# Kernel tuning notes

Measured on AMD Instinct MI355X. Metric: run time of the kernel, lower is better.

## Reference

```python
import jax, jax.numpy as jnp
import numpy as np

B_, S_, F_, N_, H_ = 4, 8192, 512, 64, 2048  # batch, seq, features, state_dim, mlp hidden
EPS = 1e-5


def setup_inputs() -> dict:
    key = jax.random.key(0)
    ks = jax.random.split(key, 24)
    F, N, H = F_, N_, H_

    def nrm(k, shape, scale=1.0):
        return jax.random.normal(k, shape, dtype=jnp.float32) * scale

    inp = {}
    inp['x'] = nrm(ks[0], (B_, S_, F))
    inp['cond'] = nrm(ks[1], (B_, F))
    n = jnp.arange(N, dtype=jnp.float32)
    for i, p in enumerate(['fwd', 'bwd']):
        b = 2 + i * 6
        inp[p + '_logAre'] = jnp.log(n + 0.5)          # HiPPO-diag: A_real = -(n+0.5)
        inp[p + '_Aim'] = jnp.pi * n                    # HiPPO-diag: A_imag = pi*n
        inp[p + '_Bre'] = nrm(ks[b], (N, F), 1.0 / np.sqrt(N))
        inp[p + '_Bim'] = nrm(ks[b + 1], (N, F), 1.0 / np.sqrt(N))
        inp[p + '_Cre'] = nrm(ks[b + 2], (F, N), 1.0 / np.sqrt(F))
        inp[p + '_Cim'] = nrm(ks[b + 3], (F, N), 1.0 / np.sqrt(F))
        inp[p + '_D'] = nrm(ks[b + 4], (F,))
        inp[p + '_logdt'] = jax.random.uniform(ks[b + 5], (N,), minval=jnp.log(0.001), maxval=jnp.log(0.1))
    inp['proj_w'] = nrm(ks[14], (2 * F, F), 1.0 / np.sqrt(2 * F))
    inp['proj_b'] = jnp.zeros((F,), jnp.float32)
    # AdaLN modulation: Dense(6F) on silu(cond); zero-init in the model, small random here
    inp['ada_w'] = nrm(ks[15], (F, 6 * F), 0.02)
    inp['ada_b'] = jnp.zeros((6 * F,), jnp.float32)
    inp['mlp_w1'] = nrm(ks[16], (F, H), 1.0 / np.sqrt(F))
    inp['mlp_b1'] = jnp.zeros((H,), jnp.float32)
    inp['mlp_w2'] = nrm(ks[17], (H, F), 1.0 / np.sqrt(H))
    inp['mlp_b2'] = jnp.zeros((F,), jnp.float32)
    return inp


def _ln(x):
    mu = jnp.mean(x, axis=-1, keepdims=True)
    v = jnp.mean(jnp.square(x - mu), axis=-1, keepdims=True)
    return (x - mu) * jax.lax.rsqrt(v + EPS)


def _s5(u, logAre, Aim, Bre, Bim, Cre, Cim, D, logdt):
    dt = jnp.exp(logdt)
    A = -jnp.exp(logAre) + 1j * Aim                       # [N] complex diagonal
    A_bar = jnp.exp(A * dt)                               # ZOH discretization
    B_bar = (A_bar[:, None] - 1.0) / (A[:, None] + 1e-8) * (Bre + 1j * Bim)  # [N,F]
    u32 = u.astype(jnp.float32)
    Bu = jnp.einsum('bsf,nf->bsn', u32, B_bar)            # [B,S,N] complex
    Ab = jnp.broadcast_to(A_bar[None, None, :], Bu.shape)

    def op(e1, e2):
        a1, b1 = e1
        a2, b2 = e2
        return (a1 * a2, a2 * b1 + b2)

    _, xs = jax.lax.associative_scan(op, (Ab, Bu), axis=1)
    y = jnp.einsum('fn,bsn->bsf', Cre + 1j * Cim, xs).real + D * u32
    return y.astype(u.dtype)


def reference(x, cond, fwd_logAre, fwd_Aim, fwd_Bre, fwd_Bim, fwd_Cre, fwd_Cim, fwd_D, fwd_logdt,
              bwd_logAre, bwd_Aim, bwd_Bre, bwd_Bim, bwd_Cre, bwd_Cim, bwd_D, bwd_logdt,
              proj_w, proj_b, ada_w, ada_b, mlp_w1, mlp_b1, mlp_w2, mlp_b2):
    mods = jax.nn.silu(cond) @ ada_w + ada_b              # [B,6F]
    sh1, sc1, g1, sh2, sc2, g2 = [m[:, None, :] for m in jnp.split(mods, 6, axis=-1)]
    h = _ln(x) * (1.0 + sc1) + sh1
    y_fwd = _s5(h, fwd_logAre, fwd_Aim, fwd_Bre, fwd_Bim, fwd_Cre, fwd_Cim, fwd_D, fwd_logdt)
    y_bwd = jnp.flip(_s5(jnp.flip(h, axis=1), bwd_logAre, bwd_Aim, bwd_Bre, bwd_Bim, bwd_Cre, bwd_Cim, bwd_D, bwd_logdt), axis=1)
    y = jnp.concatenate([y_fwd, y_bwd], axis=-1) @ proj_w + proj_b
    x = x + g1 * y
    h2 = _ln(x) * (1.0 + sc2) + sh2
    x = x + g2 * (jax.nn.gelu(h2 @ mlp_w1 + mlp_b1) @ mlp_w2 + mlp_b2)
    return x
```

## Files before the change

kernel.cpp:

```cpp
#include <hip/hip_runtime.h>
#include <hip/hip_bf16.h>

typedef unsigned short u16;
typedef __attribute__((ext_vector_type(8))) short bf16x8;
typedef __attribute__((ext_vector_type(4))) float f32x4;

#define Bc 4
#define Sc 8192
#define Fc 512
#define Nc 64
#define Hc 2048
#define SIXF 3072

__device__ __forceinline__ u16 f2bf(float v) {
  __hip_bfloat16 h = __float2bfloat16(v);
  return *reinterpret_cast<u16*>(&h);
}
__device__ __forceinline__ float bf2f(u16 u) {
  return __uint_as_float(((unsigned)u) << 16);
}
__device__ __forceinline__ float ldf(const void* p, long i, int bf) {
  return bf ? bf2f(((const u16*)p)[i]) : ((const float*)p)[i];
}

__device__ __forceinline__ void ld16(const u16* g, u16* l) {
  __builtin_amdgcn_global_load_lds(
      (const __attribute__((address_space(1))) unsigned int*)g,
      (__attribute__((address_space(3))) unsigned int*)l,
      16, 0, 0);
}

__device__ __forceinline__ void xcd_swz(int& bx, int& by) {
  int gx = gridDim.x;
  int nwg = gx * gridDim.y;
  int lin = blockIdx.x + gx * blockIdx.y;
  if ((nwg & 7) == 0) {
    int q = nwg >> 3;
    lin = (lin & 7) * q + (lin >> 3);
  }
  bx = lin % gx;
  by = lin / gx;
}

__global__ void k_detect(const u16* __restrict__ x, int* __restrict__ flag) {
  if (threadIdx.x == 0) {
    int cnt = 0;
    for (int i = 0; i < 256; ++i) {
      int e = (x[i] >> 7) & 0xFF;
      cnt += (e >= 130);
    }
    *flag = (cnt >= 16) ? 0 : 1;
  }
}

__global__ void k_convert(const void* __restrict__ src, float* __restrict__ dst,
                          int n, const int* __restrict__ flag) {
  int bf = *flag;
  int i = blockIdx.x * blockDim.x + threadIdx.x;
  int stride = gridDim.x * blockDim.x;
  for (int j = i; j < n; j += stride) dst[j] = ldf(src, j, bf);
}

__global__ __launch_bounds__(256) void k_mods_init(const void* __restrict__ ada_b,
                                                   const int* __restrict__ flag,
                                                   float* __restrict__ mods) {
  int bf = *flag;
  int col = blockIdx.x * 256 + threadIdx.x;
  float v = ldf(ada_b, col, bf);
  for (int b = 0; b < Bc; ++b) mods[b * SIXF + col] = v;
}

__global__ __launch_bounds__(256) void k_mods2(const void* __restrict__ cond,
                                               const void* __restrict__ ada_w,
                                               const int* __restrict__ flag,
                                               float* __restrict__ mods) {
  int bf = *flag;
  int b = blockIdx.y;
  int f0 = blockIdx.z * 128;
  int col = blockIdx.x * 256 + threadIdx.x;
  __shared__ float sc[128];
  for (int i = threadIdx.x; i < 128; i += 256) {
    float c = ldf(cond, b * Fc + f0 + i, bf);
    sc[i] = c / (1.f + expf(-c));
  }
  __syncthreads();
  float acc = 0.f;
  for (int f = 0; f < 128; ++f) acc = fmaf(sc[f], ldf(ada_w, (long)(f0 + f) * SIXF + col, bf), acc);
  atomicAdd(&mods[b * SIXF + col], acc);
}

__global__ void k_prep(const void* lAf, const void* Aif, const void* Brf, const void* Bif, const void* ldtf,
                       const void* lAb, const void* Aib, const void* Brb, const void* Bib, const void* ldtb,
                       const int* __restrict__ flag,
                       u16* __restrict__ Wbup, float* __restrict__ Abar) {
  int bf = *flag;
  int dir = blockIdx.x;
  int f0 = blockIdx.y * 64;
  int n = threadIdx.x;
  const void* lA = dir ? lAb : lAf;
  const void* Ai = dir ? Aib : Aif;
  const void* Br = dir ? Brb : Brf;
  const void* Bi = dir ? Bib : Bif;
  const void* ld = dir ? ldtb : ldtf;
  float dt  = expf(ldf(ld, n, bf));
  float Are = -expf(ldf(lA, n, bf));
  float Aim = ldf(Ai, n, bf);
  float er  = expf(Are * dt);
  float abr = er * cosf(Aim * dt);
  float abi = er * sinf(Aim * dt);
  if (blockIdx.y == 0) {
    Abar[(dir * Nc + n) * 2 + 0] = abr;
    Abar[(dir * Nc + n) * 2 + 1] = abi;
  }
  float dr = Are + 1e-8f, di = Aim;
  float den = dr * dr + di * di;
  float nr = abr - 1.f, ni = abi;
  float cr = (nr * dr + ni * di) / den;
  float ci = (ni * dr - nr * di) / den;
  int col_re = dir * 128 + n, col_im = dir * 128 + 64 + n;
  for (int f = f0; f < f0 + 64; ++f) {
    float br = ldf(Br, n * Fc + f, bf), bi = ldf(Bi, n * Fc + f, bf);
    Wbup[(((f >> 3) * 256) + col_re) * 8 + (f & 7)] = f2bf(cr * br - ci * bi);
    Wbup[(((f >> 3) * 256) + col_im) * 8 + (f & 7)] = f2bf(cr * bi + ci * br);
  }
}

__global__ __launch_bounds__(256) void k_P2p(const void* Df, const void* Db, const void* pw,
                                             const int* __restrict__ flag, u16* __restrict__ Wyp) {
  int bf = *flag;
  int idx = blockIdx.x * 256 + threadIdx.x;
  int f1 = idx >> 9, fo = idx & 511;
  float v = ldf(Df, f1, bf) * ldf(pw, (long)f1 * Fc + fo, bf) +
            ldf(Db, f1, bf) * ldf(pw, (long)(Fc + f1) * Fc + fo, bf);
  Wyp[((((f1 >> 3) + 64) * Fc) + fo) * 8 + (f1 & 7)] = f2bf(v);
}

__global__ __launch_bounds__(256) void k_Cpm(const void* Cref, const void* Cimf,
                                             const void* Creb, const void* Cimb,
                                             const int* __restrict__ flag, u16* __restrict__ Cpm) {
  int bf = *flag;
  int k = blockIdx.x;
  int dir = k >> 7, c = (k >> 6) & 1, n = k & 63;
  const void* C = dir ? (c ? Cimb : Creb) : (c ? Cimf : Cref);
  float sgn = c ? -1.f : 1.f;
  for (int f = threadIdx.x; f < Fc; f += 256)
    Cpm[k * Fc + f] = f2bf(sgn * ldf(C, (long)f * Nc + n, bf));
}

__global__ __launch_bounds__(256) void k_Wpack(const void* __restrict__ src, const int* __restrict__ flag,
                                               int log2N, u16* __restrict__ dst) {
  int bf = *flag;
  long i = (long)blockIdx.x * 256 + threadIdx.x;
  int Nn = 1 << log2N;
  long k8 = i >> log2N;
  int n = (int)(i & (Nn - 1));
  u16 tmp[8];
#pragma unroll
  for (int j = 0; j < 8; ++j)
    tmp[j] = f2bf(ldf(src, ((k8 << 3) + j) * (long)Nn + n, bf));
  *(ushort4*)(dst + i * 8)     = *(ushort4*)tmp;
  *(ushort4*)(dst + i * 8 + 4) = *(ushort4*)(tmp + 4);
}

__global__ __launch_bounds__(256) void k_ln(const void* __restrict__ src, int srcmode,
                                            long src_tok_base, int b0,
                                            const int* __restrict__ flag,
                                            const float* __restrict__ mods,
                                            int sh_base, int sc_base,
                                            u16* __restrict__ dst, int ldd, int dcol) {
  int bf = srcmode ? 1 : *flag;
  long lt = blockIdx.x;
  int b = b0 + (int)(lt >> 13);
  int t = threadIdx.x;
  long si = (src_tok_base + lt) * Fc;
  float x0 = ldf(src, si + t, bf);
  float x1 = ldf(src, si + t + 256, bf);
  float s = x0 + x1, qq = x0 * x0 + x1 * x1;
  for (int o = 32; o; o >>= 1) { s += __shfl_down(s, o); qq += __shfl_down(qq, o); }
  __shared__ float ss[4], sq[4];
  int w = t >> 6;
  if ((t & 63) == 0) { ss[w] = s; sq[w] = qq; }
  __syncthreads();
  float S = ss[0] + ss[1] + ss[2] + ss[3];
  float Q = sq[0] + sq[1] + sq[2] + sq[3];
  float mu = S * (1.f / Fc);
  float var = Q * (1.f / Fc) - mu * mu;
  float rs = rsqrtf(var + 1e-5f);
  const float* mb = mods + b * SIXF;
  float h0 = (x0 - mu) * rs * (1.f + mb[sc_base + t]) + mb[sh_base + t];
  float h1 = (x1 - mu) * rs * (1.f + mb[sc_base + t + 256]) + mb[sh_base + t + 256];
  dst[lt * (long)ldd + dcol + t] = f2bf(h0);
  dst[lt * (long)ldd + dcol + t + 256] = f2bf(h1);
}

struct SmemA { u16 As[2][128 * 64]; u16 Ws[2][64 * 128]; };

__device__ __forceinline__ void mfma_gemm128(SmemA& sm, const u16* __restrict__ A, long row0,
                                             int lda, int K,
                                             const u16* __restrict__ Wp, int N, int col0,
                                             f32x4 (&acc)[4][4]) {
  const int tid = threadIdx.x;
  const int l = tid & 63, q = l >> 4, li = l & 15;
  const int w = tid >> 6;
  const int wm = (w >> 1) << 6, wn = (w & 1) << 6;
  const int m0 = tid >> 3;
  const int kc0 = (tid & 7) ^ (m0 & 7);
  const long aoff0 = (row0 + m0) * (long)lda + (kc0 << 3);
  const long woff0 = (long)(tid >> 7) * ((long)N << 3) + ((long)(col0 + (tid & 127)) << 3);
  const int lb = w << 9;
  const int T = K >> 6;
  int cur = 0;
  auto stage = [&](int buf, int k0) {
#pragma unroll
    for (int it = 0; it < 4; ++it)
      ld16(A + aoff0 + (long)it * ((long)lda << 5) + k0, sm.As[buf] + (it << 11) + lb);
#pragma unroll
    for (int it = 0; it < 4; ++it)
      ld16(Wp + woff0 + (long)k0 * N + (long)it * ((long)N << 4), sm.Ws[buf] + (it << 11) + lb);
  };
  stage(0, 0);
  for (int t = 0; t < T; ++t) {
    if (t + 1 < T) {
      stage(cur ^ 1, (t + 1) << 6);
      asm volatile("s_waitcnt vmcnt(8)" ::: "memory");
    } else {
      asm volatile("s_waitcnt vmcnt(0)" ::: "memory");
    }
    __builtin_amdgcn_s_barrier();
    __builtin_amdgcn_sched_barrier(0);
    const u16* As = sm.As[cur];
    const u16* Ws = sm.Ws[cur];
#pragma unroll
    for (int ks = 0; ks < 2; ++ks) {
      bf16x8 af[4], bw[4];
#pragma unroll
      for (int mt = 0; mt < 4; ++mt) {
        int mrow = wm + (mt << 4) + li;
        af[mt] = *(const bf16x8*)(As + (((mrow << 3) + (((ks << 2) + q) ^ (mrow & 7))) << 3));
      }
#pragma unroll
      for (int nt = 0; nt < 4; ++nt) {
        int n = wn + (nt << 4) + li;
        bw[nt] = *(const bf16x8*)(Ws + (((((ks << 2) + q) << 7) | n) << 3));
      }
#pragma unroll
      for (int mt = 0; mt < 4; ++mt)
#pragma unroll
        for (int nt = 0; nt < 4; ++nt)
          acc[mt][nt] = __builtin_amdgcn_mfma_f32_16x16x32_bf16(af[mt], bw[nt], acc[mt][nt], 0, 0, 0);
    }
    __builtin_amdgcn_s_barrier();
    __builtin_amdgcn_sched_barrier(0);
    cur ^= 1;
  }
}

struct SmemC { u16 As[4][256 * 32]; u16 Ws[4][32 * 256]; };

__device__ __forceinline__ void mfma_gemm256(SmemC& sm, const u16* __restrict__ A, long row0,
                                             int lda, int K,
                                             const u16* __restrict__ Wp, int N, int col0,
                                             f32x4 (&acc)[8][4]) {
  const int tid = threadIdx.x;
  const int l = tid & 63, q = l >> 4, li = l & 15;
  const int w = tid >> 6;
  const int wm = (w >> 2) << 7, wn = (w & 3) << 6;
  const int m0 = tid >> 2;
  const int kc0 = (tid & 3) ^ ((tid >> 3) & 3);
  const long aoff0 = (row0 + m0) * (long)lda + (kc0 << 3);
  const long woff0 = (long)(tid >> 8) * ((long)N << 3) + ((long)(col0 + (tid & 255)) << 3);
  const int T = K >> 5;
  auto stage = [&](int buf, int t) {
    const int k0 = t << 5;
#pragma unroll
    for (int it = 0; it < 2; ++it)
      ld16(A + aoff0 + (long)(it << 7) * lda + k0, sm.As[buf] + (((it << 9) + tid) << 3));
#pragma unroll
    for (int it = 0; it < 2; ++it)
      ld16(Wp + woff0 + (((long)((k0 >> 3) + (it << 1)) * N) << 3),
           sm.Ws[buf] + (((it << 9) + tid) << 3));
  };
  stage(0, 0); stage(1, 1); stage(2, 2);
  for (int t = 0; t < T; ++t) {
    if (t + 3 < T) stage((t + 3) & 3, t + 3);
    int rem = T - 1 - t;
    if (rem >= 3)      asm volatile("s_waitcnt vmcnt(12)" ::: "memory");
    else if (rem == 2) asm volatile("s_waitcnt vmcnt(8)" ::: "memory");
    else if (rem == 1) asm volatile("s_waitcnt vmcnt(4)" ::: "memory");
    else               asm volatile("s_waitcnt vmcnt(0)" ::: "memory");
    __builtin_amdgcn_s_barrier();
    __builtin_amdgcn_sched_barrier(0);
    const u16* As = sm.As[t & 3];
    const u16* Ws = sm.Ws[t & 3];
    __builtin_amdgcn_s_setprio(1);
    bf16x8 bw[4];
#pragma unroll
    for (int nt = 0; nt < 4; ++nt) {
      int n = wn + (nt << 4) + li;
      bw[nt] = *(const bf16x8*)(Ws + (((q << 8) | n) << 3));
    }
#pragma unroll
    for (int mt = 0; mt < 8; ++mt) {
      int mrow = wm + (mt << 4) + li;
      bf16x8 af = *(const bf16x8*)(As + (((mrow << 2) + (q ^ ((mrow >> 1) & 3))) << 3));
#pragma unroll
      for (int nt = 0; nt < 4; ++nt)
        acc[mt][nt] = __builtin_amdgcn_mfma_f32_16x16x32_bf16(af, bw[nt], acc[mt][nt], 0, 0, 0);
    }
    __builtin_amdgcn_s_setprio(0);
    __builtin_amdgcn_s_barrier();
    __builtin_amdgcn_sched_barrier(0);
  }
}

__global__ __launch_bounds__(256) void k_Gp2(const u16* __restrict__ Cpm, const u16* __restrict__ pwp,
                                             u16* __restrict__ Wyp) {
  __shared__ SmemA sm;
  f32x4 acc[4][4] = {};
  int bx, by; xcd_swz(bx, by);
  long row0 = (long)by * 128;
  int col0 = bx << 7;
  int dir = (int)(row0 >> 7);
  mfma_gemm128(sm, Cpm, row0, Fc, Fc, pwp + (size_t)dir * 262144, Fc, col0, acc);
  const int l = threadIdx.x & 63, q = l >> 4, li = l & 15;
  const int w = threadIdx.x >> 6;
  const int wm = (w >> 1) << 6, wn = (w & 1) << 6;
#pragma unroll
  for (int mt = 0; mt < 4; ++mt)
#pragma unroll
    for (int nt = 0; nt < 4; ++nt)
#pragma unroll
      for (int r = 0; r < 4; ++r) {
        int k = (int)row0 + wm + (mt << 4) + (q << 2) + r;
        int col = col0 + wn + (nt << 4) + li;
        u16 v = f2bf(acc[mt][nt][r]);
        size_t i0 = (((size_t)(k >> 3)) * Fc + col) * 8 + (k & 7);
        Wyp[i0] = v;
        Wyp[i0 + (size_t)32 * Fc * 8] = v;
      }
}

__global__ __launch_bounds__(256) void k_gemm_bu(const u16* __restrict__ hp,
                                                 const u16* __restrict__ Wbup,
                                                 int nb, float* __restrict__ Bu) {
  __shared__ SmemA sm;
  f32x4 acc[4][4] = {};
  int bx, by; xcd_swz(bx, by);
  long row0 = (long)by * 128;
  int col0 = bx << 7;
  mfma_gemm128(sm, hp, row0, 1024, Fc, Wbup, 256, col0, acc);
  const int l = threadIdx.x & 63, q = l >> 4, li = l & 15;
  const int w = threadIdx.x >> 6;
  const int wm = (w >> 1) << 6, wn = (w & 1) << 6;
#pragma unroll
  for (int mt = 0; mt < 4; ++mt) {
#pragma unroll
    for (int nt = 0; nt < 4; ++nt) {
      int col = col0 + wn + (nt << 4) + li;
      int dir = col >> 7, cc = (col >> 6) & 1, n = col & 63;
#pragma unroll
      for (int r = 0; r < 4; ++r) {
        long lt = row0 + wm + (mt << 4) + (q << 2) + r;
        int lb = (int)(lt >> 13), s = (int)(lt & 8191);
        int spos = dir ? (Sc - 1 - s) : s;
        Bu[((((long)dir * nb + lb) * Nc + n) * Sc + spos) * 2 + cc] = acc[mt][nt][r];
      }
    }
  }
}

__global__ __launch_bounds__(256) void k_scan(float* __restrict__ Bu, const float* __restrict__ Abar,
                                              int nb) {
  int blk = blockIdx.x;
  int per_dir = nb * 64;
  int dir = blk / per_dir;
  int rem = blk - dir * per_dir;
  int lb = rem >> 6, n = rem & 63;
  float ar = Abar[(dir * Nc + n) * 2 + 0];
  float ai = Abar[(dir * Nc + n) * 2 + 1];
  float* base = Bu + (((long)dir * nb + lb) * Nc + n) * Sc * 2;
  int t = threadIdx.x;
  float4 loc[16];
  float lr = 0.f, li = 0.f;
  const float4* bp = (const float4*)base + t * 16;
#pragma unroll
  for (int j = 0; j < 16; ++j) {
    float4 v = bp[j];
    loc[j] = v;
    float nr = fmaf(ar, lr, fmaf(-ai, li, v.x));
    float ni = fmaf(ar, li, fmaf(ai, lr, v.y));
    lr = fmaf(ar, nr, fmaf(-ai, ni, v.z));
    li = fmaf(ar, ni, fmaf(ai, nr, v.w));
  }
  __shared__ float sr[256], si[256];
  float pr = ar, pi = ai;
  for (int k = 0; k < 5; ++k) { float t2 = pr * pr - pi * pi; pi = 2.f * pr * pi; pr = t2; }
  float vr = lr, vi = li;
  for (int step = 1; step < 256; step <<= 1) {
    sr[t] = vr; si[t] = vi;
    __syncthreads();
    if (t >= step) {
      float orr = sr[t - step], oii = si[t - step];
      vr = vr + pr * orr - pi * oii;
      vi = vi + pr * oii + pi * orr;
    }
    __syncthreads();
    float t2 = pr * pr - pi * pi; pi = 2.f * pr * pi; pr = t2;
  }
  sr[t] = vr; si[t] = vi;
  __syncthreads();
  float xr = (t == 0) ? 0.f : sr[t - 1];
  float xi = (t == 0) ? 0.f : si[t - 1];
  float4* op = (float4*)base + t * 16;
#pragma unroll
  for (int j = 0; j < 16; ++j) {
    float4 v = loc[j];
    float nr = fmaf(ar, xr, fmaf(-ai, xi, v.x));
    float ni = fmaf(ar, xi, fmaf(ai, xr, v.y));
    xr = fmaf(ar, nr, fmaf(-ai, ni, v.z));
    xi = fmaf(ar, ni, fmaf(ai, nr, v.w));
    float4 o; o.x = nr; o.y = ni; o.z = xr; o.w = xi;
    op[j] = o;
  }
}

__global__ __launch_bounds__(256) void k_xs_t(const float* __restrict__ xs, int nb,
                                              u16* __restrict__ hxl) {
  __shared__ float tile[32 * 257];
  long t0 = (long)blockIdx.x * 32;
  int lb = (int)(t0 >> 13);
  int s0 = (int)(t0 & 8191);
  int tid = threadIdx.x;
  int ls = tid & 31;
  int half = (tid >> 5) & 1;
  int wv = tid >> 6;
#pragma unroll 4
  for (int cg = 0; cg < 32; ++cg) {
    int col = cg * 8 + wv * 2 + half;
    int dir = col >> 7, cc = (col >> 6) & 1, n = col & 63;
    int spos = dir ? (Sc - 1 - (s0 + ls)) : (s0 + ls);
    float v = xs[((((long)dir * nb + lb) * Nc + n) * Sc + spos) * 2 + cc];
    tile[ls * 257 + col] = v;
  }
  __syncthreads();
  for (int j = 0; j < 32; ++j) {
    float v = tile[j * 257 + tid];
    u16 hi = f2bf(v);
    long lt = t0 + j;
    hxl[lt * 1024 + tid] = hi;
    hxl[lt * 1024 + 256 + tid] = f2bf(v - bf2f(hi));
  }
}

__global__ __launch_bounds__(512, 2) void k_gemm_y(const u16* __restrict__ hxl,
                                                   const u16* __restrict__ Wyp,
                                                   const void* __restrict__ xraw, long tok_base, int b0,
                                                   const int* __restrict__ flag,
                                                   const float* __restrict__ mods,
                                                   const float* __restrict__ pb,
                                                   u16* __restrict__ out1) {
  __shared__ SmemC sm;
  f32x4 acc[8][4] = {};
  int bx, by; xcd_swz(bx, by);
  long row0 = (long)by << 8;
  int col0 = bx << 8;
  mfma_gemm256(sm, hxl, row0, 1024, 1024, Wyp, Fc, col0, acc);
  int bf = *flag;
  const int l = threadIdx.x & 63, q = l >> 4, li = l & 15;
  const int w = threadIdx.x >> 6;
  const int wm = (w >> 2) << 7, wn = (w & 3) << 6;
#pragma unroll
  for (int mt = 0; mt < 8; ++mt) {
#pragma unroll
    for (int r = 0; r < 4; ++r) {
      long lt = row0 + wm + (mt << 4) + (q << 2) + r;
      int b = b0 + (int)(lt >> 13);
      const float* mb = mods + b * SIXF + 2 * Fc;
#pragma unroll
      for (int nt = 0; nt < 4; ++nt) {
        int col = col0 + wn + (nt << 4) + li;
        float xv = ldf(xraw, (tok_base + lt) * Fc + col, bf);
        out1[lt * Fc + col] = f2bf(xv + mb[col] * (acc[mt][nt][r] + pb[col]));
      }
    }
  }
}

__device__ __forceinline__ float gelu_t(float u) {
  float z = 0.7978845608028654f * fmaf(0.044715f * u * u, u, u);
  float e = __builtin_amdgcn_exp2f(z * -2.8853900817779268f);
  return u * __builtin_amdgcn_rcpf(1.f + e);
}

__global__ __launch_bounds__(512, 2) void k_mlp1(const u16* __restrict__ h2, const u16* __restrict__ W1p,
                                                 const float* __restrict__ b1, long crow0,
                                                 u16* __restrict__ tbuf) {
  __shared__ SmemC sm;
  f32x4 acc[8][4] = {};
  int bx, by; xcd_swz(bx, by);
  long row0 = crow0 + ((long)by << 8);
  int col0 = bx << 8;
  mfma_gemm256(sm, h2, row0, Fc, Fc, W1p, Hc, col0, acc);
  const int l = threadIdx.x & 63, q = l >> 4, li = l & 15;
  const int w = threadIdx.x >> 6;
  const int wm = (w >> 2) << 7, wn = (w & 3) << 6;
#pragma unroll
  for (int mt = 0; mt < 8; ++mt) {
#pragma unroll
    for (int r = 0; r < 4; ++r) {
      long lr2 = row0 - crow0 + wm + (mt << 4) + (q << 2) + r;
#pragma unroll
      for (int nt = 0; nt < 4; ++nt) {
        int col = col0 + wn + (nt << 4) + li;
        tbuf[lr2 * Hc + col] = f2bf(gelu_t(acc[mt][nt][r] + b1[col]));
      }
    }
  }
}

__global__ __launch_bounds__(256) void k_mlp2(const u16* __restrict__ tbuf, const u16* __restrict__ W2p,
                                              const float* __restrict__ b2, const u16* __restrict__ out1,
                                              const float* __restrict__ mods, long crow0,
                                              long tok_base, int b0,
                                              const int* __restrict__ flag, void* __restrict__ dout) {
  __shared__ SmemA sm;
  f32x4 acc[4][4] = {};
  int bx, by; xcd_swz(bx, by);
  long lrow0 = (long)by * 128;
  int col0 = bx << 7;
  mfma_gemm128(sm, tbuf, lrow0, Hc, Hc, W2p, Fc, col0, acc);
  int bf = *flag;
  const int l = threadIdx.x & 63, q = l >> 4, li = l & 15;
  const int w = threadIdx.x >> 6;
  const int wm = (w >> 1) << 6, wn = (w & 1) << 6;
#pragma unroll
  for (int mt = 0; mt < 4; ++mt) {
#pragma unroll
    for (int r = 0; r < 4; ++r) {
      long lt = crow0 + lrow0 + wm + (mt << 4) + (q << 2) + r;
      int b = b0 + (int)(lt >> 13);
      const float* mb = mods + b * SIXF + 5 * Fc;
#pragma unroll
      for (int nt = 0; nt < 4; ++nt) {
        int col = col0 + wn + (nt << 4) + li;
        float v = bf2f(out1[lt * Fc + col]) + mb[col] * (acc[mt][nt][r] + b2[col]);
        long oi = (tok_base + lt) * Fc + col;
        if (bf) ((u16*)dout)[oi] = f2bf(v);
        else    ((float*)dout)[oi] = v;
      }
    }
  }
}

extern "C" void kernel_launch(void* const* d_in, const int* in_sizes, int n_in,
                              void* d_out, int out_size, void* d_ws, size_t ws_size,
                              hipStream_t stream) {
  char* ws = (char*)d_ws;
  size_t off = 0;
  auto alloc = [&](size_t bytes) -> char* {
    char* p = ws + off;
    off += (bytes + 255) & ~(size_t)255;
    return p;
  };
  int*   flag = (int*)  alloc(4);
  float* mods = (float*)alloc((size_t)Bc * SIXF * 4);
  float* Abar = (float*)alloc(2 * Nc * 2 * 4);
  float* pbf  = (float*)alloc(Fc * 4);
  float* b1f  = (float*)alloc(Hc * 4);
  float* b2f  = (float*)alloc(Fc * 4);
  u16* Wbup = (u16*)alloc((size_t)Fc * 256 * 2);
  u16* Wyp  = (u16*)alloc((size_t)128 * Fc * 8 * 2);
  u16* W1p  = (u16*)alloc((size_t)Fc * Hc * 2);
  u16* W2p  = (u16*)alloc((size_t)Hc * Fc * 2);
  u16* pwp  = (u16*)alloc((size_t)1024 * Fc * 2);
  u16* Cpm  = (u16*)alloc((size_t)256 * Fc * 2);
  size_t off_static = off;

  const size_t U = (size_t)Sc * Fc * 2;
  int nb = 4;
  while (nb > 1 && off_static + (size_t)nb * 4 * U + 4096 > ws_size) nb >>= 1;

  u16*   hxl  = (u16*)  alloc((size_t)nb * U * 2);
  float* Bu   = (float*)alloc((size_t)nb * U);
  u16*   out1 = (u16*)  alloc((size_t)nb * U);
  u16* tch = hxl;
  u16* h2  = (u16*)Bu;

  k_detect<<<1, 64, 0, stream>>>((const u16*)d_in[0], flag);
  k_convert<<<2, 256, 0, stream>>>(d_in[19], pbf, Fc, flag);
  k_convert<<<8, 256, 0, stream>>>(d_in[23], b1f, Hc, flag);
  k_convert<<<2, 256, 0, stream>>>(d_in[25], b2f, Fc, flag);
  k_mods_init<<<12, 256, 0, stream>>>(d_in[21], flag, mods);
  k_mods2<<<dim3(12, Bc, 4), 256, 0, stream>>>(d_in[1], d_in[20], flag, mods);
  k_prep<<<dim3(2, 8), 64, 0, stream>>>(d_in[2], d_in[3], d_in[4], d_in[5], d_in[9],
                                        d_in[10], d_in[11], d_in[12], d_in[13], d_in[17],
                                        flag, Wbup, Abar);
  k_P2p<<<(Fc * Fc) / 256, 256, 0, stream>>>(d_in[8], d_in[16], d_in[18], flag, Wyp);
  k_Wpack<<<256, 256, 0, stream>>>(d_in[18], flag, 9, pwp);
  k_Cpm<<<256, 256, 0, stream>>>(d_in[6], d_in[7], d_in[14], d_in[15], flag, Cpm);
  k_Gp2<<<dim3(4, 2), 256, 0, stream>>>(Cpm, pwp, Wyp);
  k_Wpack<<<512, 256, 0, stream>>>(d_in[22], flag, 11, W1p);
  k_Wpack<<<512, 256, 0, stream>>>(d_in[24], flag, 9, W2p);

  for (int b0 = 0; b0 < Bc; b0 += nb) {
    long tok_base = (long)b0 * Sc;
    long rows = (long)nb * Sc;
    k_ln<<<rows, 256, 0, stream>>>(d_in[0], 0, tok_base, b0, flag, mods, 0, Fc, hxl, 1024, 512);
    k_gemm_bu<<<dim3(2, rows / 128), 256, 0, stream>>>(hxl + 512, Wbup, nb, Bu);
    k_scan<<<2 * nb * 64, 256, 0, stream>>>(Bu, Abar, nb);
    k_xs_t<<<rows / 32, 256, 0, stream>>>(Bu, nb, hxl);
    k_gemm_y<<<dim3(2, rows / 256), 512, 0, stream>>>(hxl, Wyp, d_in[0], tok_base, b0,
                                                      flag, mods, pbf, out1);
    k_ln<<<rows, 256, 0, stream>>>(out1, 1, 0, b0, flag, mods, 3 * Fc, 4 * Fc, h2, 512, 0);
    long RC = rows / 2;
    for (int ch = 0; ch < 2; ++ch) {
      long crow0 = ch * RC;
      k_mlp1<<<dim3(8, RC / 256), 512, 0, stream>>>(h2, W1p, b1f, crow0, tch);
      k_mlp2<<<dim3(4, RC / 128), 256, 0, stream>>>(tch, W2p, b2f, out1, mods, crow0,
                                                    tok_base, b0, flag, d_out);
    }
  }
  (void)n_in; (void)out_size; (void)in_sizes;
}
```

Before: 621.6 us.

## Restructure GEMM pipelines to one barrier per K-step and add BK=64 MLP1 path

Each GEMM main loop now waits for its loads, issues a single barrier, and only then starts the next prefetch, dropping the trailing barrier per iteration. In the 128 GEMM the prefetch is no longer overlapped with the wait because it waits on vmcnt(0). A new 256x256 GEMM with BK=64 and double buffering (128 KB of shared memory) is added for the MLP1 kernel, replacing the 4-stage BK=32 pipeline there. The larger LDS footprint may keep two blocks per CU from fitting, and the shallower prefetch can expose memory latency.

After: 628.4 us. Within noise of the previous version (+1.1%).

```diff
diff --git a/kernel.cpp b/kernel.cpp
--- a/kernel.cpp
+++ b/kernel.cpp
@@ -193,6 +193,7 @@
   dst[lt * (long)ldd + dcol + t + 256] = f2bf(h1);
 }
 
+
 struct SmemA { u16 As[2][128 * 64]; u16 Ws[2][64 * 128]; };
 
 __device__ __forceinline__ void mfma_gemm128(SmemA& sm, const u16* __restrict__ A, long row0,
@@ -220,14 +221,10 @@
   };
   stage(0, 0);
   for (int t = 0; t < T; ++t) {
-    if (t + 1 < T) {
-      stage(cur ^ 1, (t + 1) << 6);
-      asm volatile("s_waitcnt vmcnt(8)" ::: "memory");
-    } else {
-      asm volatile("s_waitcnt vmcnt(0)" ::: "memory");
-    }
+    asm volatile("s_waitcnt vmcnt(0)" ::: "memory");
     __builtin_amdgcn_s_barrier();
     __builtin_amdgcn_sched_barrier(0);
+    if (t + 1 < T) stage(cur ^ 1, (t + 1) << 6);
     const u16* As = sm.As[cur];
     const u16* Ws = sm.Ws[cur];
 #pragma unroll
@@ -249,18 +246,72 @@
         for (int nt = 0; nt < 4; ++nt)
           acc[mt][nt] = __builtin_amdgcn_mfma_f32_16x16x32_bf16(af[mt], bw[nt], acc[mt][nt], 0, 0, 0);
     }
+    cur ^= 1;
+  }
+}
+
+struct SmemB { u16 As[2][256 * 64]; u16 Ws[2][64 * 256]; };
+
+__device__ __forceinline__ void mfma_gemm256b(SmemB& sm, const u16* __restrict__ A, long row0,
+                                              int lda, int K,
+                                              const u16* __restrict__ Wp, int N, int col0,
+                                              f32x4 (&acc)[8][4]) {
+  const int tid = threadIdx.x;
+  const int l = tid & 63, q = l >> 4, li = l & 15;
+  const int w = tid >> 6;
+  const int wm = (w >> 2) << 7, wn = (w & 3) << 6;
+  const int m0 = tid >> 3;
+  const int kc0 = (tid & 7) ^ (m0 & 7);
+  const long aoff0 = (row0 + m0) * (long)lda + (kc0 << 3);
+  const long woff0 = (long)(tid >> 8) * ((long)N << 3) + ((long)(col0 + (tid & 255)) << 3);
+  const int lb = w << 9;
+  const int T = K >> 6;
+  int cur = 0;
+  auto stage = [&](int buf, int k0) {
+#pragma unroll
+    for (int it = 0; it < 4; ++it)
+      ld16(A + aoff0 + (long)it * ((long)lda << 6) + k0, sm.As[buf] + (it << 12) + lb);
+#pragma unroll
+    for (int it = 0; it < 4; ++it)
+      ld16(Wp + woff0 + (long)k0 * N + (long)it * ((long)N << 4), sm.Ws[buf] + (it << 12) + lb);
+  };
+  stage(0, 0);
+  for (int t = 0; t < T; ++t) {
+    asm volatile("s_waitcnt vmcnt(0)" ::: "memory");
     __builtin_amdgcn_s_barrier();
     __builtin_amdgcn_sched_barrier(0);
+    if (t + 1 < T) stage(cur ^ 1, (t + 1) << 6);
+    const u16* As = sm.As[cur];
+    const u16* Ws = sm.Ws[cur];
+    __builtin_amdgcn_s_setprio(1);
+#pragma unroll
+    for (int ks = 0; ks < 2; ++ks) {
+      bf16x8 bw[4];
+#pragma unroll
+      for (int nt = 0; nt < 4; ++nt) {
+        int n = wn + (nt << 4) + li;
+        bw[nt] = *(const bf16x8*)(Ws + (((((ks << 2) + q) << 8) | n) << 3));
+      }
+#pragma unroll
+      for (int mt = 0; mt < 8; ++mt) {
+        int mrow = wm + (mt << 4) + li;
+        bf16x8 af = *(const bf16x8*)(As + (((mrow << 3) + (((ks << 2) + q) ^ (mrow & 7))) << 3));
+#pragma unroll
+        for (int nt = 0; nt < 4; ++nt)
+          acc[mt][nt] = __builtin_amdgcn_mfma_f32_16x16x32_bf16(af, bw[nt], acc[mt][nt], 0, 0, 0);
+      }
+    }
+    __builtin_amdgcn_s_setprio(0);
     cur ^= 1;
   }
 }
 
 struct SmemC { u16 As[4][256 * 32]; u16 Ws[4][32 * 256]; };
 
-__device__ __forceinline__ void mfma_gemm256(SmemC& sm, const u16* __restrict__ A, long row0,
-                                             int lda, int K,
-                                             const u16* __restrict__ Wp, int N, int col0,
-                                             f32x4 (&acc)[8][4]) {
+__device__ __forceinline__ void mfma_gemm256c(SmemC& sm, const u16* __restrict__ A, long row0,
+                                              int lda, int K,
+                                              const u16* __restrict__ Wp, int N, int col0,
+                                              f32x4 (&acc)[8][4]) {
   const int tid = threadIdx.x;
   const int l = tid & 63, q = l >> 4, li = l & 15;
   const int w = tid >> 6;
@@ -282,14 +333,13 @@
   };
   stage(0, 0); stage(1, 1); stage(2, 2);
   for (int t = 0; t < T; ++t) {
-    if (t + 3 < T) stage((t + 3) & 3, t + 3);
     int rem = T - 1 - t;
-    if (rem >= 3)      asm volatile("s_waitcnt vmcnt(12)" ::: "memory");
-    else if (rem == 2) asm volatile("s_waitcnt vmcnt(8)" ::: "memory");
+    if (rem >= 2)      asm volatile("s_waitcnt vmcnt(8)" ::: "memory");
     else if (rem == 1) asm volatile("s_waitcnt vmcnt(4)" ::: "memory");
     else               asm volatile("s_waitcnt vmcnt(0)" ::: "memory");
     __builtin_amdgcn_s_barrier();
     __builtin_amdgcn_sched_barrier(0);
+    if (t + 3 < T) stage((t + 3) & 3, t + 3);
     const u16* As = sm.As[t & 3];
     const u16* Ws = sm.Ws[t & 3];
     __builtin_amdgcn_s_setprio(1);
@@ -308,8 +358,6 @@
         acc[mt][nt] = __builtin_amdgcn_mfma_f32_16x16x32_bf16(af, bw[nt], acc[mt][nt], 0, 0, 0);
     }
     __builtin_amdgcn_s_setprio(0);
-    __builtin_amdgcn_s_barrier();
-    __builtin_amdgcn_sched_barrier(0);
   }
 }
 
@@ -464,7 +512,7 @@
   int bx, by; xcd_swz(bx, by);
   long row0 = (long)by << 8;
   int col0 = bx << 8;
-  mfma_gemm256(sm, hxl, row0, 1024, 1024, Wyp, Fc, col0, acc);
+  mfma_gemm256c(sm, hxl, row0, 1024, 1024, Wyp, Fc, col0, acc);
   int bf = *flag;
   const int l = threadIdx.x & 63, q = l >> 4, li = l & 15;
   const int w = threadIdx.x >> 6;
@@ -495,12 +543,12 @@
 __global__ __launch_bounds__(512, 2) void k_mlp1(const u16* __restrict__ h2, const u16* __restrict__ W1p,
                                                  const float* __restrict__ b1, long crow0,
                                                  u16* __restrict__ tbuf) {
-  __shared__ SmemC sm;
+  __shared__ SmemB sm;
   f32x4 acc[8][4] = {};
   int bx, by; xcd_swz(bx, by);
   long row0 = crow0 + ((long)by << 8);
   int col0 = bx << 8;
-  mfma_gemm256(sm, h2, row0, Fc, Fc, W1p, Hc, col0, acc);
+  mfma_gemm256b(sm, h2, row0, Fc, Fc, W1p, Hc, col0, acc);
   const int l = threadIdx.x & 63, q = l >> 4, li = l & 15;
   const int w = threadIdx.x >> 6;
   const int wm = (w >> 2) << 7, wn = (w & 3) << 6;
```

## Shrink big GEMM tiles to 128x256 with triple buffering and single barrier

Applied to the files above, without the earlier changes.

Replaces the 256x256 tile, 512-thread GEMM used by the y-projection and first MLP layer with a 128x256 tile on 256 threads, where each wave owns a 64-column strip across all 128 rows. It uses a 3-deep LDS ring with the next stage issued after the barrier, and drops the trailing barrier per K step. The 128x128 GEMM loop is also reordered: it waits for all loads, barriers, then prefetches the next buffer, so one barrier per iteration is removed. The aim is less barrier overhead and smaller LDS per block for better occupancy. The cost is less reuse per tile and, in the 128 GEMM, a full vmcnt(0) wait that serialises load and compute more.

New measurement: 624.5 us. No clear change (+0.5%).

```diff
diff --git a/kernel.cpp b/kernel.cpp
--- a/kernel.cpp
+++ b/kernel.cpp
@@ -193,6 +193,7 @@
   dst[lt * (long)ldd + dcol + t + 256] = f2bf(h1);
 }
 
+
 struct SmemA { u16 As[2][128 * 64]; u16 Ws[2][64 * 128]; };
 
 __device__ __forceinline__ void mfma_gemm128(SmemA& sm, const u16* __restrict__ A, long row0,
@@ -220,14 +221,10 @@
   };
   stage(0, 0);
   for (int t = 0; t < T; ++t) {
-    if (t + 1 < T) {
-      stage(cur ^ 1, (t + 1) << 6);
-      asm volatile("s_waitcnt vmcnt(8)" ::: "memory");
-    } else {
-      asm volatile("s_waitcnt vmcnt(0)" ::: "memory");
-    }
+    asm volatile("s_waitcnt vmcnt(0)" ::: "memory");
     __builtin_amdgcn_s_barrier();
     __builtin_amdgcn_sched_barrier(0);
+    if (t + 1 < T) stage(cur ^ 1, (t + 1) << 6);
     const u16* As = sm.As[cur];
     const u16* Ws = sm.Ws[cur];
 #pragma unroll
@@ -249,49 +246,44 @@
         for (int nt = 0; nt < 4; ++nt)
           acc[mt][nt] = __builtin_amdgcn_mfma_f32_16x16x32_bf16(af[mt], bw[nt], acc[mt][nt], 0, 0, 0);
     }
-    __builtin_amdgcn_s_barrier();
-    __builtin_amdgcn_sched_barrier(0);
     cur ^= 1;
   }
 }
 
-struct SmemC { u16 As[4][256 * 32]; u16 Ws[4][32 * 256]; };
-
-__device__ __forceinline__ void mfma_gemm256(SmemC& sm, const u16* __restrict__ A, long row0,
-                                             int lda, int K,
-                                             const u16* __restrict__ Wp, int N, int col0,
-                                             f32x4 (&acc)[8][4]) {
+struct SmemD { u16 As[3][128 * 32]; u16 Ws[3][32 * 256]; };
+
+__device__ __forceinline__ void mfma_gemmD(SmemD& sm, const u16* __restrict__ A, long row0,
+                                           int lda, int K,
+                                           const u16* __restrict__ Wp, int N, int col0,
+                                           f32x4 (&acc)[8][4]) {
   const int tid = threadIdx.x;
   const int l = tid & 63, q = l >> 4, li = l & 15;
   const int w = tid >> 6;
-  const int wm = (w >> 2) << 7, wn = (w & 3) << 6;
+  const int wn = w << 6;
   const int m0 = tid >> 2;
   const int kc0 = (tid & 3) ^ ((tid >> 3) & 3);
   const long aoff0 = (row0 + m0) * (long)lda + (kc0 << 3);
-  const long woff0 = (long)(tid >> 8) * ((long)N << 3) + ((long)(col0 + (tid & 255)) << 3);
+  const long woff0 = ((long)(col0 + tid)) << 3;
   const int T = K >> 5;
   auto stage = [&](int buf, int t) {
     const int k0 = t << 5;
-#pragma unroll
-    for (int it = 0; it < 2; ++it)
-      ld16(A + aoff0 + (long)(it << 7) * lda + k0, sm.As[buf] + (((it << 9) + tid) << 3));
-#pragma unroll
-    for (int it = 0; it < 2; ++it)
-      ld16(Wp + woff0 + (((long)((k0 >> 3) + (it << 1)) * N) << 3),
-           sm.Ws[buf] + (((it << 9) + tid) << 3));
+    ld16(A + aoff0 + k0, sm.As[buf] + (tid << 3));
+    ld16(A + aoff0 + ((long)lda << 6) + k0, sm.As[buf] + ((tid + 256) << 3));
+#pragma unroll
+    for (int j = 0; j < 4; ++j)
+      ld16(Wp + woff0 + (((long)((k0 >> 3) + j) * N) << 3),
+           sm.Ws[buf] + (((j << 8) + tid) << 3));
   };
-  stage(0, 0); stage(1, 1); stage(2, 2);
+  stage(0, 0);
+  if (T > 1) stage(1, 1);
   for (int t = 0; t < T; ++t) {
-    if (t + 3 < T) stage((t + 3) & 3, t + 3);
-    int rem = T - 1 - t;
-    if (rem >= 3)      asm volatile("s_waitcnt vmcnt(12)" ::: "memory");
-    else if (rem == 2) asm volatile("s_waitcnt vmcnt(8)" ::: "memory");
-    else if (rem == 1) asm volatile("s_waitcnt vmcnt(4)" ::: "memory");
-    else               asm volatile("s_waitcnt vmcnt(0)" ::: "memory");
+    if (t + 1 < T) asm volatile("s_waitcnt vmcnt(6)" ::: "memory");
+    else           asm volatile("s_waitcnt vmcnt(0)" ::: "memory");
     __builtin_amdgcn_s_barrier();
     __builtin_amdgcn_sched_barrier(0);
-    const u16* As = sm.As[t & 3];
-    const u16* Ws = sm.Ws[t & 3];
+    if (t + 2 < T) stage((t + 2) % 3, t + 2);
+    const u16* As = sm.As[t % 3];
+    const u16* Ws = sm.Ws[t % 3];
     __builtin_amdgcn_s_setprio(1);
     bf16x8 bw[4];
 #pragma unroll
@@ -301,15 +293,13 @@
     }
 #pragma unroll
     for (int mt = 0; mt < 8; ++mt) {
-      int mrow = wm + (mt << 4) + li;
+      int mrow = (mt << 4) + li;
       bf16x8 af = *(const bf16x8*)(As + (((mrow << 2) + (q ^ ((mrow >> 1) & 3))) << 3));
 #pragma unroll
       for (int nt = 0; nt < 4; ++nt)
         acc[mt][nt] = __builtin_amdgcn_mfma_f32_16x16x32_bf16(af, bw[nt], acc[mt][nt], 0, 0, 0);
     }
     __builtin_amdgcn_s_setprio(0);
-    __builtin_amdgcn_s_barrier();
-    __builtin_amdgcn_sched_barrier(0);
   }
 }
 
@@ -452,28 +442,27 @@
   }
 }
 
-__global__ __launch_bounds__(512, 2) void k_gemm_y(const u16* __restrict__ hxl,
+__global__ __launch_bounds__(256, 2) void k_gemm_y(const u16* __restrict__ hxl,
                                                    const u16* __restrict__ Wyp,
                                                    const void* __restrict__ xraw, long tok_base, int b0,
                                                    const int* __restrict__ flag,
                                                    const float* __restrict__ mods,
                                                    const float* __restrict__ pb,
                                                    u16* __restrict__ out1) {
-  __shared__ SmemC sm;
+  __shared__ SmemD sm;
   f32x4 acc[8][4] = {};
   int bx, by; xcd_swz(bx, by);
-  long row0 = (long)by << 8;
+  long row0 = (long)by << 7;
   int col0 = bx << 8;
-  mfma_gemm256(sm, hxl, row0, 1024, 1024, Wyp, Fc, col0, acc);
+  mfma_gemmD(sm, hxl, row0, 1024, 1024, Wyp, Fc, col0, acc);
   int bf = *flag;
   const int l = threadIdx.x & 63, q = l >> 4, li = l & 15;
-  const int w = threadIdx.x >> 6;
-  const int wm = (w >> 2) << 7, wn = (w & 3) << 6;
+  const int wn = (threadIdx.x >> 6) << 6;
 #pragma unroll
   for (int mt = 0; mt < 8; ++mt) {
 #pragma unroll
     for (int r = 0; r < 4; ++r) {
-      long lt = row0 + wm + (mt << 4) + (q << 2) + r;
+      long lt = row0 + (mt << 4) + (q << 2) + r;
       int b = b0 + (int)(lt >> 13);
       const float* mb = mods + b * SIXF + 2 * Fc;
 #pragma unroll
@@ -492,23 +481,22 @@
   return u * __builtin_amdgcn_rcpf(1.f + e);
 }
 
-__global__ __launch_bounds__(512, 2) void k_mlp1(const u16* __restrict__ h2, const u16* __restrict__ W1p,
+__global__ __launch_bounds__(256, 2) void k_mlp1(const u16* __restrict__ h2, const u16* __restrict__ W1p,
                                                  const float* __restrict__ b1, long crow0,
                                                  u16* __restrict__ tbuf) {
-  __shared__ SmemC sm;
+  __shared__ SmemD sm;
   f32x4 acc[8][4] = {};
   int bx, by; xcd_swz(bx, by);
-  long row0 = crow0 + ((long)by << 8);
+  long row0 = crow0 + ((long)by << 7);
   int col0 = bx << 8;
-  mfma_gemm256(sm, h2, row0, Fc, Fc, W1p, Hc, col0, acc);
+  mfma_gemmD(sm, h2, row0, Fc, Fc, W1p, Hc, col0, acc);
   const int l = threadIdx.x & 63, q = l >> 4, li = l & 15;
-  const int w = threadIdx.x >> 6;
-  const int wm = (w >> 2) << 7, wn = (w & 3) << 6;
+  const int wn = (threadIdx.x >> 6) << 6;
 #pragma unroll
   for (int mt = 0; mt < 8; ++mt) {
 #pragma unroll
     for (int r = 0; r < 4; ++r) {
-      long lr2 = row0 - crow0 + wm + (mt << 4) + (q << 2) + r;
+      long lr2 = row0 - crow0 + (mt << 4) + (q << 2) + r;
 #pragma unroll
       for (int nt = 0; nt < 4; ++nt) {
         int col = col0 + wn + (nt << 4) + li;
@@ -609,13 +597,13 @@
     k_gemm_bu<<<dim3(2, rows / 128), 256, 0, stream>>>(hxl + 512, Wbup, nb, Bu);
     k_scan<<<2 * nb * 64, 256, 0, stream>>>(Bu, Abar, nb);
     k_xs_t<<<rows / 32, 256, 0, stream>>>(Bu, nb, hxl);
-    k_gemm_y<<<dim3(2, rows / 256), 512, 0, stream>>>(hxl, Wyp, d_in[0], tok_base, b0,
+    k_gemm_y<<<dim3(2, rows / 128), 256, 0, stream>>>(hxl, Wyp, d_in[0], tok_base, b0,
                                                       flag, mods, pbf, out1);
     k_ln<<<rows, 256, 0, stream>>>(out1, 1, 0, b0, flag, mods, 3 * Fc, 4 * Fc, h2, 512, 0);
     long RC = rows / 2;
     for (int ch = 0; ch < 2; ++ch) {
       long crow0 = ch * RC;
-      k_mlp1<<<dim3(8, RC / 256), 512, 0, stream>>>(h2, W1p, b1f, crow0, tch);
+      k_mlp1<<<dim3(8, RC / 128), 256, 0, stream>>>(h2, W1p, b1f, crow0, tch);
       k_mlp2<<<dim3(4, RC / 128), 256, 0, stream>>>(tch, W2p, b2f, out1, mods, crow0,
                                                     tok_base, b0, flag, d_out);
     }
```
